# Optimization experiments

Hardware: AMD Instinct MI355X
Metric: run time of the kernel (lower is better)

The kernel has to match this reference:

```python
import jax, jax.numpy as jnp
import numpy as np

N, D, K = 262144, 64, 1024

def setup_inputs() -> dict:
    key = jax.random.key(0)
    kx, ke = jax.random.split(key)
    x = jax.random.normal(kx, (N, D), dtype=jnp.float32)
    # nn.Embedding weight initialized uniform(-1, 1)
    emb = jax.random.uniform(ke, (K, D), dtype=jnp.float32, minval=-1.0, maxval=1.0)
    return {"x": x, "emb": emb}

def reference(x, emb):
    # x: [N, D], emb: [K, D]
    xf = x.reshape(-1, emb.shape[1])
    x2 = jnp.sum(xf * xf, axis=-1, keepdims=True)          # [N, 1]
    e2 = jnp.sum(emb * emb, axis=-1)                        # [K]
    xe = jnp.einsum('nd,kd->nk', xf, emb)                   # [N, K]
    dist = jnp.sqrt(jnp.maximum(x2 + e2 - 2.0 * xe, 0.0))   # [N, K], matches torch.cdist p=2
    indices = jnp.argmin(dist, axis=-1)[None, :]             # [1, N] (cdist had batch dim 1)
    quantized = emb[indices[0]].reshape(xf.shape)            # [N, D]
    return quantized, indices
```

## Files before the change

### kernel.cpp

```cpp
#include <hip/hip_runtime.h>

#define NPTS 262144
#define DIM 64
#define KCODES 1024

typedef short bf16x8 __attribute__((ext_vector_type(8)));
typedef float f32x4 __attribute__((ext_vector_type(4)));
typedef short short8 __attribute__((ext_vector_type(8)));

#define GTILE_BYTES 393216
#define E2_OFF (GTILE_BYTES)

__device__ __forceinline__ unsigned short bf16_rne(float v) {
    unsigned int u = __float_as_uint(v);
    return (unsigned short)((u + 0x7FFFu + ((u >> 16) & 1u)) >> 16);
}
__device__ __forceinline__ float bf16_to_f32(unsigned short h) {
    return __uint_as_float(((unsigned int)h) << 16);
}

__global__ void vq_e2_kernel(const float* __restrict__ emb, float* __restrict__ e2) {
    int k = blockIdx.x * blockDim.x + threadIdx.x;
    if (k < KCODES) {
        const float4* row = reinterpret_cast<const float4*>(emb + k * DIM);
        float s = 0.f;
#pragma unroll
        for (int j = 0; j < DIM / 4; ++j) {
            float4 v = row[j];
            s = fmaf(v.x, v.x, s);
            s = fmaf(v.y, v.y, s);
            s = fmaf(v.z, v.z, s);
            s = fmaf(v.w, v.w, s);
        }
        e2[k] = s;
    }
}

__global__ void vq_tile_kernel(const float* __restrict__ emb, unsigned short* __restrict__ gtile) {
    int t = blockIdx.x * blockDim.x + threadIdx.x;
    if (t >= 64 * 3 * 2 * 64) return;
    int kc = t / 384;
    int r = t % 384;
    int s = r / 128;
    int r2 = r % 128;
    int chunk = r2 / 64;
    int l = r2 % 64;
    int code = kc * 16 + (l & 15);
    int dim0 = chunk * 32 + (l >> 4) * 8;
    const float* src = emb + code * DIM + dim0;
    short8 out;
#pragma unroll
    for (int e = 0; e < 8; ++e) {
        float v = -2.f * src[e];
        unsigned short hs = bf16_rne(v);
        float rr = v - bf16_to_f32(hs);
        unsigned short ms = bf16_rne(rr);
        float rr2 = rr - bf16_to_f32(ms);
        unsigned short ls = bf16_rne(rr2);
        out[e] = (short)((s == 0) ? hs : ((s == 1) ? ms : ls));
    }
    *reinterpret_cast<short8*>(gtile + (size_t)t * 8) = out;
}

__global__ __launch_bounds__(256, 2) void vq_mfma_kernel(
    const float* __restrict__ x, const unsigned short* __restrict__ gtile,
    const float* __restrict__ e2g, float* __restrict__ candout) {
    __shared__ __align__(16) unsigned short etile[24576];
    __shared__ float e2s[128];

    const int tid = threadIdx.x;
    const int lane = tid & 63;
    const int wid = tid >> 6;
    const int ptbase = blockIdx.x * 128 + wid * 32;
    const int c16 = lane & 15;
    const int hi = lane >> 4;

    bf16x8 ah[2][2], am[2][2], al[2][2];
#pragma unroll
    for (int T = 0; T < 2; ++T) {
#pragma unroll
        for (int c = 0; c < 2; ++c) {
            const float* src = x + (size_t)(ptbase + T * 16 + c16) * DIM + c * 32 + hi * 8;
            float4 f0 = *reinterpret_cast<const float4*>(src);
            float4 f1 = *reinterpret_cast<const float4*>(src + 4);
            float va[8] = {f0.x, f0.y, f0.z, f0.w, f1.x, f1.y, f1.z, f1.w};
            bf16x8 vh, vm, vl;
#pragma unroll
            for (int e = 0; e < 8; ++e) {
                float v = va[e];
                unsigned short hs = bf16_rne(v);
                float rr = v - bf16_to_f32(hs);
                unsigned short ms = bf16_rne(rr);
                float rr2 = rr - bf16_to_f32(ms);
                unsigned short ls = bf16_rne(rr2);
                vh[e] = (short)hs; vm[e] = (short)ms; vl[e] = (short)ls;
            }
            ah[T][c] = vh; am[T][c] = vm; al[T][c] = vl;
        }
    }

    float b1[2][4], b2[2][4];
    int i1[2][4], i2[2][4];
#pragma unroll
    for (int T = 0; T < 2; ++T)
#pragma unroll
        for (int r = 0; r < 4; ++r) { b1[T][r] = 3.4e38f; b2[T][r] = 3.4e38f; i1[T][r] = 0; i2[T][r] = 0; }

    for (int R = 0; R < 8; ++R) {
        const bf16x8* g8 = reinterpret_cast<const bf16x8*>(gtile) + R * 3072;
        bf16x8* l8 = reinterpret_cast<bf16x8*>(etile);
#pragma unroll
        for (int j = 0; j < 12; ++j) l8[tid + j * 256] = g8[tid + j * 256];
        if (tid < 128) e2s[tid] = e2g[R * 128 + tid];
        __syncthreads();

#pragma unroll
        for (int kcL = 0; kcL < 8; ++kcL) {
            const int code_c = R * 128 + kcL * 16 + c16;
            const float e2v = e2s[kcL * 16 + c16];
            f32x4 c0[2], c1[2];
#pragma unroll
            for (int T = 0; T < 2; ++T) {
                c0[T] = (f32x4){e2v, e2v, e2v, e2v};
                c1[T] = (f32x4){0.f, 0.f, 0.f, 0.f};
            }
#pragma unroll
            for (int es = 0; es < 3; ++es) {
                const bf16x8* fb0 = reinterpret_cast<const bf16x8*>(etile + ((kcL * 3 + es) * 2 + 0) * 512);
                const bf16x8* fb1 = reinterpret_cast<const bf16x8*>(etile + ((kcL * 3 + es) * 2 + 1) * 512);
                bf16x8 bC0 = fb0[lane];
                bf16x8 bC1 = fb1[lane];
                if (es == 0) {
#pragma unroll
                    for (int T = 0; T < 2; ++T) {
                        c0[T] = __builtin_amdgcn_mfma_f32_16x16x32_bf16(ah[T][0], bC0, c0[T], 0, 0, 0);
                        c1[T] = __builtin_amdgcn_mfma_f32_16x16x32_bf16(ah[T][1], bC1, c1[T], 0, 0, 0);
                        c0[T] = __builtin_amdgcn_mfma_f32_16x16x32_bf16(am[T][0], bC0, c0[T], 0, 0, 0);
                        c1[T] = __builtin_amdgcn_mfma_f32_16x16x32_bf16(am[T][1], bC1, c1[T], 0, 0, 0);
                        c0[T] = __builtin_amdgcn_mfma_f32_16x16x32_bf16(al[T][0], bC0, c0[T], 0, 0, 0);
                        c1[T] = __builtin_amdgcn_mfma_f32_16x16x32_bf16(al[T][1], bC1, c1[T], 0, 0, 0);
                    }
                } else if (es == 1) {
#pragma unroll
                    for (int T = 0; T < 2; ++T) {
                        c0[T] = __builtin_amdgcn_mfma_f32_16x16x32_bf16(ah[T][0], bC0, c0[T], 0, 0, 0);
                        c1[T] = __builtin_amdgcn_mfma_f32_16x16x32_bf16(ah[T][1], bC1, c1[T], 0, 0, 0);
                        c0[T] = __builtin_amdgcn_mfma_f32_16x16x32_bf16(am[T][0], bC0, c0[T], 0, 0, 0);
                        c1[T] = __builtin_amdgcn_mfma_f32_16x16x32_bf16(am[T][1], bC1, c1[T], 0, 0, 0);
                    }
                } else {
#pragma unroll
                    for (int T = 0; T < 2; ++T) {
                        c0[T] = __builtin_amdgcn_mfma_f32_16x16x32_bf16(ah[T][0], bC0, c0[T], 0, 0, 0);
                        c1[T] = __builtin_amdgcn_mfma_f32_16x16x32_bf16(ah[T][1], bC1, c1[T], 0, 0, 0);
                    }
                }
            }
#pragma unroll
            for (int T = 0; T < 2; ++T) {
#pragma unroll
                for (int r = 0; r < 4; ++r) {
                    float s = c0[T][r] + c1[T][r];
                    bool lt1 = s < b1[T][r];
                    bool lt2 = s < b2[T][r];
                    i2[T][r] = lt1 ? i1[T][r] : (lt2 ? code_c : i2[T][r]);
                    b2[T][r] = lt1 ? b1[T][r] : (lt2 ? s : b2[T][r]);
                    i1[T][r] = lt1 ? code_c : i1[T][r];
                    b1[T][r] = lt1 ? s : b1[T][r];
                }
            }
        }
        __syncthreads();
    }

#pragma unroll
    for (int T = 0; T < 2; ++T) {
#pragma unroll
        for (int r = 0; r < 4; ++r) {
#pragma unroll
            for (int mask = 1; mask <= 8; mask <<= 1) {
                float q1 = __shfl_xor(b1[T][r], mask);
                int qi1 = __shfl_xor(i1[T][r], mask);
                float q2 = __shfl_xor(b2[T][r], mask);
                int qi2 = __shfl_xor(i2[T][r], mask);
                bool qbest = (q1 < b1[T][r]) || (q1 == b1[T][r] && qi1 < i1[T][r]);
                float c2a = qbest ? b1[T][r] : b2[T][r];
                int c2ai = qbest ? i1[T][r] : i2[T][r];
                float c2b = qbest ? q2 : q1;
                int c2bi = qbest ? qi2 : qi1;
                bool bsec = (c2b < c2a) || (c2b == c2a && c2bi < c2ai);
                b1[T][r] = qbest ? q1 : b1[T][r];
                i1[T][r] = qbest ? qi1 : i1[T][r];
                b2[T][r] = bsec ? c2b : c2a;
                i2[T][r] = bsec ? c2bi : c2ai;
            }
        }
    }
    if (c16 == 0) {
#pragma unroll
        for (int T = 0; T < 2; ++T)
#pragma unroll
            for (int r = 0; r < 4; ++r) {
                unsigned int packed = (unsigned int)i1[T][r] | ((unsigned int)i2[T][r] << 10);
                candout[ptbase + T * 16 + hi * 4 + r] = __uint_as_float(packed);
            }
    }
}

__global__ void vq_rescue_kernel(const float* __restrict__ x, const float* __restrict__ emb,
                                 const float* __restrict__ e2,
                                 float* __restrict__ qout, float* __restrict__ iout) {
    const size_t p = (size_t)blockIdx.x * blockDim.x + threadIdx.x;
    unsigned int cw = __float_as_uint(iout[p]);
    int ca = (int)(cw & 1023u);
    int cb = (int)((cw >> 10) & 1023u);
    const float4* xrow = reinterpret_cast<const float4*>(x + p * DIM);
    const float4* ea = reinterpret_cast<const float4*>(emb + (size_t)ca * DIM);
    const float4* eb = reinterpret_cast<const float4*>(emb + (size_t)cb * DIM);
    float a0 = 0.f, a1 = 0.f, a2 = 0.f, a3 = 0.f;
    float d0 = 0.f, d1 = 0.f, d2 = 0.f, d3 = 0.f;
#pragma unroll
    for (int j = 0; j < DIM / 4; ++j) {
        float4 xv = xrow[j];
        float4 va = ea[j];
        float4 vb = eb[j];
        a0 = fmaf(xv.x, va.x, a0);
        a1 = fmaf(xv.y, va.y, a1);
        a2 = fmaf(xv.z, va.z, a2);
        a3 = fmaf(xv.w, va.w, a3);
        d0 = fmaf(xv.x, vb.x, d0);
        d1 = fmaf(xv.y, vb.y, d1);
        d2 = fmaf(xv.z, vb.z, d2);
        d3 = fmaf(xv.w, vb.w, d3);
    }
    float sa = fmaf(-2.f, (a0 + a1) + (a2 + a3), e2[ca]);
    float sb = fmaf(-2.f, (d0 + d1) + (d2 + d3), e2[cb]);
    bool bwins = (sb < sa) || (sb == sa && cb < ca);
    int win = bwins ? cb : ca;

    const float4* qrow = reinterpret_cast<const float4*>(emb + (size_t)win * DIM);
    float4* orow = reinterpret_cast<float4*>(qout + p * DIM);
#pragma unroll
    for (int j = 0; j < DIM / 4; ++j) orow[j] = qrow[j];
    iout[p] = (float)win;
}

extern "C" void kernel_launch(void* const* d_in, const int* in_sizes, int n_in,
                              void* d_out, int out_size, void* d_ws, size_t ws_size,
                              hipStream_t stream) {
    const float* x = (const float*)d_in[0];
    const float* emb = (const float*)d_in[1];
    float* qout = (float*)d_out;
    float* iout = (float*)d_out + (size_t)NPTS * DIM;

    unsigned short* gtile = (unsigned short*)d_ws;
    float* e2g = (float*)((char*)d_ws + E2_OFF);

    vq_e2_kernel<<<(KCODES + 255) / 256, 256, 0, stream>>>(emb, e2g);
    vq_tile_kernel<<<(64 * 3 * 2 * 64 + 255) / 256, 256, 0, stream>>>(emb, gtile);
    vq_mfma_kernel<<<NPTS / 128, 256, 0, stream>>>(x, gtile, e2g, iout);
    vq_rescue_kernel<<<NPTS / 256, 256, 0, stream>>>(x, emb, e2g, qout, iout);
}
```

Before: 352.2 us.

## Halve LDS code tile, preload all e2, single accumulator chain, med3 top-2 update

The codebook tile staged in LDS shrinks from 128 to 64 codes per round, doubling the number of rounds, and all 1024 e2 values are loaded into shared memory once up front. The two split-K accumulators are merged into one MFMA chain per tile, which removes a per-element add. The top-2 tracking now uses fmed3/fminf. The smaller LDS footprint may allow more blocks per CU, at the cost of more barriers, and the single dependent MFMA chain may expose more accumulator latency.

```diff
diff --git a/kernel.cpp b/kernel.cpp
--- a/kernel.cpp
+++ b/kernel.cpp
@@ -65,8 +65,8 @@
 __global__ __launch_bounds__(256, 2) void vq_mfma_kernel(
     const float* __restrict__ x, const unsigned short* __restrict__ gtile,
     const float* __restrict__ e2g, float* __restrict__ candout) {
-    __shared__ __align__(16) unsigned short etile[24576];
-    __shared__ float e2s[128];
+    __shared__ __align__(16) unsigned short etile[12288];
+    __shared__ float e2all[KCODES];
 
     const int tid = threadIdx.x;
     const int lane = tid & 63;
@@ -99,6 +99,9 @@
         }
     }
 
+#pragma unroll
+    for (int i = 0; i < 4; ++i) e2all[tid + i * 256] = e2g[tid + i * 256];
+
     float b1[2][4], b2[2][4];
     int i1[2][4], i2[2][4];
 #pragma unroll
@@ -106,53 +109,50 @@
 #pragma unroll
         for (int r = 0; r < 4; ++r) { b1[T][r] = 3.4e38f; b2[T][r] = 3.4e38f; i1[T][r] = 0; i2[T][r] = 0; }
 
-    for (int R = 0; R < 8; ++R) {
-        const bf16x8* g8 = reinterpret_cast<const bf16x8*>(gtile) + R * 3072;
+    const bf16x8* etile_v = reinterpret_cast<const bf16x8*>(etile);
+
+    for (int R2 = 0; R2 < 16; ++R2) {
+        __syncthreads();
+        const bf16x8* g8 = reinterpret_cast<const bf16x8*>(gtile) + R2 * 1536;
         bf16x8* l8 = reinterpret_cast<bf16x8*>(etile);
 #pragma unroll
-        for (int j = 0; j < 12; ++j) l8[tid + j * 256] = g8[tid + j * 256];
-        if (tid < 128) e2s[tid] = e2g[R * 128 + tid];
+        for (int j = 0; j < 6; ++j) l8[tid + j * 256] = g8[tid + j * 256];
         __syncthreads();
 
 #pragma unroll
-        for (int kcL = 0; kcL < 8; ++kcL) {
-            const int code_c = R * 128 + kcL * 16 + c16;
-            const float e2v = e2s[kcL * 16 + c16];
-            f32x4 c0[2], c1[2];
-#pragma unroll
-            for (int T = 0; T < 2; ++T) {
-                c0[T] = (f32x4){e2v, e2v, e2v, e2v};
-                c1[T] = (f32x4){0.f, 0.f, 0.f, 0.f};
-            }
+        for (int kcL = 0; kcL < 4; ++kcL) {
+            const int code_c = R2 * 64 + kcL * 16 + c16;
+            const float e2v = e2all[code_c];
+            f32x4 c[2];
+            c[0] = (f32x4){e2v, e2v, e2v, e2v};
+            c[1] = c[0];
 #pragma unroll
             for (int es = 0; es < 3; ++es) {
-                const bf16x8* fb0 = reinterpret_cast<const bf16x8*>(etile + ((kcL * 3 + es) * 2 + 0) * 512);
-                const bf16x8* fb1 = reinterpret_cast<const bf16x8*>(etile + ((kcL * 3 + es) * 2 + 1) * 512);
-                bf16x8 bC0 = fb0[lane];
-                bf16x8 bC1 = fb1[lane];
+                bf16x8 bc0 = etile_v[(kcL * 6 + es * 2 + 0) * 64 + lane];
+                bf16x8 bc1 = etile_v[(kcL * 6 + es * 2 + 1) * 64 + lane];
                 if (es == 0) {
 #pragma unroll
                     for (int T = 0; T < 2; ++T) {
-                        c0[T] = __builtin_amdgcn_mfma_f32_16x16x32_bf16(ah[T][0], bC0, c0[T], 0, 0, 0);
-                        c1[T] = __builtin_amdgcn_mfma_f32_16x16x32_bf16(ah[T][1], bC1, c1[T], 0, 0, 0);
-                        c0[T] = __builtin_amdgcn_mfma_f32_16x16x32_bf16(am[T][0], bC0, c0[T], 0, 0, 0);
-                        c1[T] = __builtin_amdgcn_mfma_f32_16x16x32_bf16(am[T][1], bC1, c1[T], 0, 0, 0);
-                        c0[T] = __builtin_amdgcn_mfma_f32_16x16x32_bf16(al[T][0], bC0, c0[T], 0, 0, 0);
-                        c1[T] = __builtin_amdgcn_mfma_f32_16x16x32_bf16(al[T][1], bC1, c1[T], 0, 0, 0);
+                        c[T] = __builtin_amdgcn_mfma_f32_16x16x32_bf16(ah[T][0], bc0, c[T], 0, 0, 0);
+                        c[T] = __builtin_amdgcn_mfma_f32_16x16x32_bf16(ah[T][1], bc1, c[T], 0, 0, 0);
+                        c[T] = __builtin_amdgcn_mfma_f32_16x16x32_bf16(am[T][0], bc0, c[T], 0, 0, 0);
+                        c[T] = __builtin_amdgcn_mfma_f32_16x16x32_bf16(am[T][1], bc1, c[T], 0, 0, 0);
+                        c[T] = __builtin_amdgcn_mfma_f32_16x16x32_bf16(al[T][0], bc0, c[T], 0, 0, 0);
+                        c[T] = __builtin_amdgcn_mfma_f32_16x16x32_bf16(al[T][1], bc1, c[T], 0, 0, 0);
                     }
                 } else if (es == 1) {
 #pragma unroll
                     for (int T = 0; T < 2; ++T) {
-                        c0[T] = __builtin_amdgcn_mfma_f32_16x16x32_bf16(ah[T][0], bC0, c0[T], 0, 0, 0);
-                        c1[T] = __builtin_amdgcn_mfma_f32_16x16x32_bf16(ah[T][1], bC1, c1[T], 0, 0, 0);
-                        c0[T] = __builtin_amdgcn_mfma_f32_16x16x32_bf16(am[T][0], bC0, c0[T], 0, 0, 0);
-                        c1[T] = __builtin_amdgcn_mfma_f32_16x16x32_bf16(am[T][1], bC1, c1[T], 0, 0, 0);
+                        c[T] = __builtin_amdgcn_mfma_f32_16x16x32_bf16(ah[T][0], bc0, c[T], 0, 0, 0);
+                        c[T] = __builtin_amdgcn_mfma_f32_16x16x32_bf16(ah[T][1], bc1, c[T], 0, 0, 0);
+                        c[T] = __builtin_amdgcn_mfma_f32_16x16x32_bf16(am[T][0], bc0, c[T], 0, 0, 0);
+                        c[T] = __builtin_amdgcn_mfma_f32_16x16x32_bf16(am[T][1], bc1, c[T], 0, 0, 0);
                     }
                 } else {
 #pragma unroll
                     for (int T = 0; T < 2; ++T) {
-                        c0[T] = __builtin_amdgcn_mfma_f32_16x16x32_bf16(ah[T][0], bC0, c0[T], 0, 0, 0);
-                        c1[T] = __builtin_amdgcn_mfma_f32_16x16x32_bf16(ah[T][1], bC1, c1[T], 0, 0, 0);
+                        c[T] = __builtin_amdgcn_mfma_f32_16x16x32_bf16(ah[T][0], bc0, c[T], 0, 0, 0);
+                        c[T] = __builtin_amdgcn_mfma_f32_16x16x32_bf16(ah[T][1], bc1, c[T], 0, 0, 0);
                     }
                 }
             }
@@ -160,17 +160,16 @@
             for (int T = 0; T < 2; ++T) {
 #pragma unroll
                 for (int r = 0; r < 4; ++r) {
-                    float s = c0[T][r] + c1[T][r];
+                    float s = c[T][r];
                     bool lt1 = s < b1[T][r];
                     bool lt2 = s < b2[T][r];
-                    i2[T][r] = lt1 ? i1[T][r] : (lt2 ? code_c : i2[T][r]);
-                    b2[T][r] = lt1 ? b1[T][r] : (lt2 ? s : b2[T][r]);
+                    i2[T][r] = lt2 ? (lt1 ? i1[T][r] : code_c) : i2[T][r];
+                    b2[T][r] = __builtin_amdgcn_fmed3f(b1[T][r], s, b2[T][r]);
                     i1[T][r] = lt1 ? code_c : i1[T][r];
-                    b1[T][r] = lt1 ? s : b1[T][r];
+                    b1[T][r] = fminf(s, b1[T][r]);
                 }
             }
         }
-        __syncthreads();
     }
 
 #pragma unroll
```

After: 362.0 us. 2.8% more time.
